# Optimization experiments

Measured on AMD Instinct MI355X. Metric: run time of the kernel, lower is better.

The kernel has to match this reference:

```python
import jax, jax.numpy as jnp
import numpy as np

N_TOK, D_MODEL, N_EXPERTS, TOP_K = 8192, 512, 8, 2


def setup_inputs() -> dict:
    key = jax.random.key(0)
    k1, k2, k3 = jax.random.split(key, 3)
    x = jax.random.normal(k1, (N_TOK, D_MODEL), jnp.float32)
    w_gate = jax.random.normal(k2, (D_MODEL, N_EXPERTS), jnp.float32) * 0.02
    expert_w = jax.random.normal(k3, (N_EXPERTS, D_MODEL, D_MODEL), jnp.float32) * (D_MODEL ** -0.5)
    return {"x": x, "w_gate": w_gate, "expert_w": expert_w, "top_k": TOP_K}


def _cv_sq(v):
    m = jnp.mean(v)
    return jnp.var(v) / (m * m + 1e-10)


def reference(x, w_gate, expert_w, top_k):
    # ---- Gate (clean top-k gating, eval mode of noisy-top-k) ----
    logits = x @ w_gate                              # [N, E]
    top_vals, top_idx = jax.lax.top_k(logits, top_k)  # [N, k]
    top_gates = jax.nn.softmax(top_vals, axis=-1)
    n, e = logits.shape
    gates = jnp.zeros((n, e), x.dtype).at[jnp.arange(n)[:, None], top_idx].set(top_gates)

    # ---- dispatch -> per-expert GEMM -> log-domain combine ----
    # combine(): stitched = cat(expert_out).exp() * nonzero_gates; index_add over
    # batch index; zeros -> eps; log. Dense-equivalent (tokens with gate 0
    # contribute exactly nothing):
    expert_out = jnp.einsum('nd,edf->nef', x, expert_w)   # per-expert outputs [N, E, D]
    combined = jnp.einsum('ne,nef->nf', gates, jnp.exp(expert_out))  # [N, D]
    eps = np.float32(np.finfo(np.float64).eps)
    combined = jnp.where(combined == 0, eps, combined)
    out = jnp.log(combined)

    # ---- load-balance aux loss: cv^2(importance) + cv^2(load) ----
    importance = gates.sum(0)
    load = (gates > 0).sum(0).astype(x.dtype)
    balance_loss = _cv_sq(importance) + _cv_sq(load)
    return out, balance_loss
```

## Files before the change

### kernel.cpp

```cpp
#include <hip/hip_runtime.h>
#include <hip/hip_bf16.h>
#include <math.h>

#define N_TOK 8192
#define D 512
#define NE 8

typedef float f32x4 __attribute__((ext_vector_type(4)));
typedef __bf16 bf16x8 __attribute__((ext_vector_type(8)));
typedef unsigned short u16;
typedef u16 u16x8 __attribute__((ext_vector_type(8)));

#define OFF_TOKG  65792
#define OFF_BUCK  131328
#define OFF_XB    (1u << 20)
#define OFF_EWT   (OFF_XB + 8u * 1024 * 1024)
#define OFF_Y     (OFF_EWT + 4u * 1024 * 1024)

__device__ __forceinline__ u16 f2b(float v) {
    __hip_bfloat16 h = __float2bfloat16(v);
    return *reinterpret_cast<u16*>(&h);
}
__device__ __forceinline__ float b2f(u16 u) {
    __hip_bfloat16 h;
    *reinterpret_cast<u16*>(&h) = u;
    return __bfloat162float(h);
}

typedef __attribute__((address_space(1))) const void* gp1_t;
typedef __attribute__((address_space(3))) void* lp3_t;
__device__ __forceinline__ void gload16(const void* g, void* l) {
    __builtin_amdgcn_global_load_lds((gp1_t)g, (lp3_t)l, 16, 0, 0);
}

__global__ __launch_bounds__(256) void gate_prep_kernel(
    const float* __restrict__ x, const float* __restrict__ wg,
    const float* __restrict__ ew,
    float* __restrict__ tok_g, u16* __restrict__ xb, u16* __restrict__ ewt,
    int* __restrict__ count, float* __restrict__ imp, int* __restrict__ bucket)
{
    __shared__ __align__(16) float sbuf[64 * 65];
    int b = blockIdx.x;
    int tid = threadIdx.x;

    if (b >= 512) {
        int pb = b - 512;
        float (*tile)[65] = (float(*)[65])sbuf;
        int e = pb >> 6, dt = (pb >> 3) & 7, ftl = pb & 7;
        int c = tid & 63, rq = tid >> 6;
        const float* src = ew + (size_t)e * D * D + (size_t)(dt * 64) * D + ftl * 64;
#pragma unroll
        for (int i = 0; i < 16; ++i) {
            int r = i * 4 + rq;
            tile[r][c] = src[(size_t)r * D + c];
        }
        __syncthreads();
        u16* dst = ewt + (size_t)e * D * D + (size_t)(ftl * 64) * D + dt * 64;
#pragma unroll
        for (int i = 0; i < 16; ++i) {
            int f = i * 4 + rq;
            dst[(size_t)f * D + c] = f2b(tile[c][f]);
        }
        return;
    }

    __shared__ int lcnt[NE], lbase[NE];
    __shared__ float limp[NE];
    __shared__ int se[32], so[32];
    if (tid < NE) { lcnt[tid] = 0; limp[tid] = 0.f; }

    float* wgs = sbuf;
    for (int i = tid; i < NE * D; i += 256) {
        int d = i >> 3, e = i & 7;
        wgs[e * D + d] = wg[i];
    }
    __syncthreads();

    int wave = tid >> 6, lane = tid & 63;
#pragma unroll
    for (int t = 0; t < 4; ++t) {
        int n = b * 16 + wave * 4 + t;
        const float4* xr4 = (const float4*)(x + (size_t)n * D);
        ushort4* xb4 = (ushort4*)(xb + (size_t)n * D);

        float p[NE];
#pragma unroll
        for (int e = 0; e < NE; ++e) p[e] = 0.f;
#pragma unroll
        for (int it = 0; it < 2; ++it) {
            float4 v = xr4[it * 64 + lane];
            ushort4 s;
            s.x = f2b(v.x); s.y = f2b(v.y); s.z = f2b(v.z); s.w = f2b(v.w);
            xb4[it * 64 + lane] = s;
#pragma unroll
            for (int e = 0; e < NE; ++e) {
                float4 wv = *(const float4*)&wgs[e * D + (it * 64 + lane) * 4];
                p[e] += v.x * wv.x + v.y * wv.y + v.z * wv.z + v.w * wv.w;
            }
        }
#pragma unroll
        for (int off = 32; off > 0; off >>= 1) {
#pragma unroll
            for (int e = 0; e < NE; ++e)
                p[e] += __shfl_xor(p[e], off);
        }

        if (lane == 0) {
            int e1 = 0; float v1 = p[0];
#pragma unroll
            for (int e = 1; e < NE; ++e) if (p[e] > v1) { v1 = p[e]; e1 = e; }
            int e2 = -1; float v2 = -INFINITY;
#pragma unroll
            for (int e = 0; e < NE; ++e) if (e != e1 && p[e] > v2) { v2 = p[e]; e2 = e; }
            float tv = __expf(v2 - v1);
            float inv = 1.f / (1.f + tv);
            float g1 = inv, g2 = tv * inv;
            tok_g[2 * n] = g1;    tok_g[2 * n + 1] = g2;
            int slot = wave * 4 + t;
            int o1 = atomicAdd(&lcnt[e1], 1);
            int o2 = atomicAdd(&lcnt[e2], 1);
            atomicAdd(&limp[e1], g1);
            atomicAdd(&limp[e2], g2);
            se[2 * slot] = e1;     so[2 * slot] = o1;
            se[2 * slot + 1] = e2; so[2 * slot + 1] = o2;
        }
    }
    __syncthreads();
    if (tid < NE) {
        lbase[tid] = atomicAdd(&count[tid], lcnt[tid]);
        atomicAdd(&imp[tid], limp[tid]);
    }
    __syncthreads();
    if (tid < 32) {
        int n = b * 16 + (tid >> 1);
        int e = se[tid];
        bucket[e * N_TOK + lbase[e] + so[tid]] = 2 * n + (tid & 1);
    }
}

__global__ __launch_bounds__(256) void moe_gemm(
    const u16* __restrict__ xb, const u16* __restrict__ ewt,
    const int* __restrict__ count, const int* __restrict__ bucket,
    u16* __restrict__ y)
{
    int b = blockIdx.x;
    int ft = b & 3;
    int tt = (b >> 2) & 63;
    int e  = b >> 8;
    int cnt = count[e];
    if (tt * 128 >= cnt) return;

    __shared__ int sl[128];
    __shared__ __align__(16) u16 smem[24576];

    int tid = threadIdx.x;
    if (tid < 128) {
        int idx = tt * 128 + tid;
        sl[tid] = (idx < cnt) ? bucket[e * N_TOK + idx] : -1;
    }
    __syncthreads();

    int w = tid >> 6, l = tid & 63;
    int c8 = (l & 3) * 8;
    int r0 = w * 32 + (l >> 2);
    int r1 = r0 + 16;
    int s0 = sl[r0], s1 = sl[r1];
    int ta0 = (s0 < 0) ? 0 : (s0 >> 1);
    int ta1 = (s1 < 0) ? 0 : (s1 >> 1);
    const u16* gA0 = xb + (size_t)ta0 * D + c8;
    const u16* gA1 = xb + (size_t)ta1 * D + c8;
    const u16* gB0 = ewt + ((size_t)e * D + ft * 128 + r0) * D + c8;
    const u16* gB1 = ewt + ((size_t)e * D + ft * 128 + r1) * D + c8;

    int wm = w & 1, wn = w >> 1;
    int lm = l & 15, quad = l >> 4, kq = quad * 8;

    f32x4 acc[4][4] = {};

    auto stage = [&](int p, int kc) {
        u16* As = smem + p * 8192;
        u16* Bs = As + 4096;
        gload16(gA0 + kc * 32, &As[(w * 32) * 32]);
        gload16(gA1 + kc * 32, &As[(w * 32 + 16) * 32]);
        gload16(gB0 + kc * 32, &Bs[(w * 32) * 32]);
        gload16(gB1 + kc * 32, &Bs[(w * 32 + 16) * 32]);
    };

    stage(0, 0);
    stage(1, 1);
    int bi = 0, bj = 2;
    for (int kc = 0; kc < 16; ++kc) {
        if (kc < 15)
            asm volatile("s_waitcnt vmcnt(4) lgkmcnt(0)" ::: "memory");
        else
            asm volatile("s_waitcnt vmcnt(0) lgkmcnt(0)" ::: "memory");
        __builtin_amdgcn_s_barrier();
        asm volatile("" ::: "memory");

        if (kc < 14) {
            stage(bj, kc + 2);
            bj = (bj == 2) ? 0 : bj + 1;
        }

        const u16* As = smem + bi * 8192;
        const u16* Bs = As + 4096;
        bi = (bi == 2) ? 0 : bi + 1;

        bf16x8 af[4], bfv[4];
#pragma unroll
        for (int i = 0; i < 4; ++i)
            af[i] = *(const bf16x8*)&As[(wm * 64 + i * 16 + lm) * 32 + kq];
#pragma unroll
        for (int j = 0; j < 4; ++j)
            bfv[j] = *(const bf16x8*)&Bs[(wn * 64 + j * 16 + lm) * 32 + kq];

        __builtin_amdgcn_s_setprio(1);
#pragma unroll
        for (int i = 0; i < 4; ++i)
#pragma unroll
            for (int j = 0; j < 4; ++j)
                acc[i][j] = __builtin_amdgcn_mfma_f32_16x16x32_bf16(
                    af[i], bfv[j], acc[i][j], 0, 0, 0);
        __builtin_amdgcn_s_setprio(0);
    }

    __syncthreads();
    u16* Es = smem + w * 2304;
#pragma unroll
    for (int h = 0; h < 2; ++h) {
#pragma unroll
        for (int i2 = 0; i2 < 2; ++i2) {
            int i = h * 2 + i2;
#pragma unroll
            for (int j = 0; j < 4; ++j)
#pragma unroll
                for (int r = 0; r < 4; ++r)
                    Es[(i2 * 16 + quad * 4 + r) * 72 + j * 16 + lm] =
                        f2b(acc[i][j][r]);
        }
        int row = l >> 1, hc = l & 1;
        int s = sl[wm * 64 + h * 32 + row];
        const u16* src = Es + row * 72 + hc * 32;
        u16* dst = y + (size_t)((s < 0) ? 0 : s) * D + ft * 128 + wn * 64 + hc * 32;
        if (s >= 0) {
#pragma unroll
            for (int c = 0; c < 4; ++c)
                *(u16x8*)(dst + c * 8) = *(const u16x8*)(src + c * 8);
        }
        __syncthreads();
    }
}

__global__ __launch_bounds__(256) void combine_kernel(
    const u16* __restrict__ y, const float* __restrict__ tok_g,
    const int* __restrict__ count, const float* __restrict__ imp,
    float* __restrict__ out)
{
    if (blockIdx.x == 2048) {
        if (threadIdx.x < 64) {
            int lane = threadIdx.x;
            float ci = (lane < NE) ? imp[lane] : 0.f;
            float cl = (lane < NE) ? (float)count[lane] : 0.f;
            float si = ci, sl2 = cl;
#pragma unroll
            for (int off = 4; off >= 1; off >>= 1) {
                si += __shfl_xor(si, off);
                sl2 += __shfl_xor(sl2, off);
            }
            float mi = si * 0.125f, ml = sl2 * 0.125f;
            float di = ci - mi, dl = cl - ml;
            float vi = (lane < NE) ? di * di : 0.f;
            float vl = (lane < NE) ? dl * dl : 0.f;
#pragma unroll
            for (int off = 4; off >= 1; off >>= 1) {
                vi += __shfl_xor(vi, off);
                vl += __shfl_xor(vl, off);
            }
            if (lane == 0) {
                vi *= 0.125f; vl *= 0.125f;
                out[N_TOK * D] = vi / (mi * mi + 1e-10f) + vl / (ml * ml + 1e-10f);
            }
        }
        return;
    }
    int idx = blockIdx.x * 256 + threadIdx.x;
    int n = idx >> 6;
    int c = (idx & 63) * 8;
    const u16x8 ua = *(const u16x8*)(y + (size_t)(2 * n) * D + c);
    const u16x8 ub = *(const u16x8*)(y + (size_t)(2 * n + 1) * D + c);
    float g1 = tok_g[2 * n], g2 = tok_g[2 * n + 1];
    const float eps = 2.2204460492503131e-16f;
    float r[8];
#pragma unroll
    for (int k = 0; k < 8; ++k) {
        float v = g1 * __expf(b2f(ua[k])) + g2 * __expf(b2f(ub[k]));
        r[k] = __logf(v == 0.f ? eps : v);
    }
    float* o = out + (size_t)n * D + c;
    *(float4*)o       = make_float4(r[0], r[1], r[2], r[3]);
    *(float4*)(o + 4) = make_float4(r[4], r[5], r[6], r[7]);
}

extern "C" void kernel_launch(void* const* d_in, const int* in_sizes, int n_in,
                              void* d_out, int out_size, void* d_ws, size_t ws_size,
                              hipStream_t stream)
{
    const float* x  = (const float*)d_in[0];
    const float* wg = (const float*)d_in[1];
    const float* ew = (const float*)d_in[2];
    char* ws = (char*)d_ws;
    int*   count  = (int*)(ws + 0);
    float* imp    = (float*)(ws + 64);
    float* tok_g  = (float*)(ws + OFF_TOKG);
    int*   bucket = (int*)(ws + OFF_BUCK);
    u16*   xb     = (u16*)(ws + OFF_XB);
    u16*   ewt    = (u16*)(ws + OFF_EWT);
    u16*   y      = (u16*)(ws + OFF_Y);
    float* out    = (float*)d_out;

    hipMemsetAsync(ws, 0, 128, stream);
    gate_prep_kernel<<<512 + 512, 256, 0, stream>>>(x, wg, ew, tok_g, xb, ewt,
                                                    count, imp, bucket);
    moe_gemm<<<NE * 64 * 4, 256, 0, stream>>>(xb, ewt, count, bucket, y);
    combine_kernel<<<2049, 256, 0, stream>>>(y, tok_g, count, imp, out);
}
```

Baseline: 125.5 us.

## Fuse gate, GEMM and combine into one cooperative persistent kernel with grid syncs

Replaces the three separate launches (gate/prep, per-expert GEMM, combine) with a single cooperative persistent kernel. It loops over work units in each phase and separates the phases with grid.sync(). The aim is to remove the launch overhead and tail gaps between kernels. The grid is sized from the occupancy query, capped at 2048 blocks, and the old launches remain as a fallback. The costs are grid-wide barriers and the register and occupancy limits of one fused kernel.

```diff
diff --git a/kernel.cpp b/kernel.cpp
--- a/kernel.cpp
+++ b/kernel.cpp
@@ -1,6 +1,9 @@
 #include <hip/hip_runtime.h>
+#include <hip/hip_cooperative_groups.h>
 #include <hip/hip_bf16.h>
 #include <math.h>
+
+namespace cg = cooperative_groups;
 
 #define N_TOK 8192
 #define D 512
@@ -31,6 +34,273 @@
 typedef __attribute__((address_space(3))) void* lp3_t;
 __device__ __forceinline__ void gload16(const void* g, void* l) {
     __builtin_amdgcn_global_load_lds((gp1_t)g, (lp3_t)l, 16, 0, 0);
+}
+
+__global__ __launch_bounds__(256, 3) void moe_mega(
+    const float* __restrict__ x, const float* __restrict__ wg,
+    const float* __restrict__ ew,
+    float* __restrict__ tok_g, u16* __restrict__ xb, u16* __restrict__ ewt,
+    int* __restrict__ count, float* __restrict__ imp, int* __restrict__ bucket,
+    u16* __restrict__ y, float* __restrict__ out)
+{
+    cg::grid_group grid = cg::this_grid();
+    const int tid = threadIdx.x;
+    const int G = gridDim.x;
+
+    __shared__ __align__(16) u16 smem[24576];
+    __shared__ int sl[128];
+    __shared__ int lcnt[NE], lbase[NE];
+    __shared__ float limp[NE];
+    __shared__ int se[32], so[32];
+
+    const int w = tid >> 6, l = tid & 63;
+
+    for (int u = blockIdx.x; u < 768; u += G) {
+        __syncthreads();
+        if (u < 512) {
+            float* wgs = (float*)smem;
+            if (tid < NE) { lcnt[tid] = 0; limp[tid] = 0.f; }
+            for (int i = tid; i < NE * D; i += 256) {
+                int d = i >> 3, e = i & 7;
+                wgs[e * D + d] = wg[i];
+            }
+            __syncthreads();
+
+#pragma unroll
+            for (int t = 0; t < 4; ++t) {
+                int n = u * 16 + w * 4 + t;
+                const float4* xr4 = (const float4*)(x + (size_t)n * D);
+                ushort4* xb4 = (ushort4*)(xb + (size_t)n * D);
+
+                float p[NE];
+#pragma unroll
+                for (int e = 0; e < NE; ++e) p[e] = 0.f;
+#pragma unroll
+                for (int it = 0; it < 2; ++it) {
+                    float4 v = xr4[it * 64 + l];
+                    ushort4 s;
+                    s.x = f2b(v.x); s.y = f2b(v.y); s.z = f2b(v.z); s.w = f2b(v.w);
+                    xb4[it * 64 + l] = s;
+#pragma unroll
+                    for (int e = 0; e < NE; ++e) {
+                        float4 wv = *(const float4*)&wgs[e * D + (it * 64 + l) * 4];
+                        p[e] += v.x * wv.x + v.y * wv.y + v.z * wv.z + v.w * wv.w;
+                    }
+                }
+#pragma unroll
+                for (int off = 32; off > 0; off >>= 1) {
+#pragma unroll
+                    for (int e = 0; e < NE; ++e)
+                        p[e] += __shfl_xor(p[e], off);
+                }
+
+                if (l == 0) {
+                    int e1 = 0; float v1 = p[0];
+#pragma unroll
+                    for (int e = 1; e < NE; ++e) if (p[e] > v1) { v1 = p[e]; e1 = e; }
+                    int e2 = -1; float v2 = -INFINITY;
+#pragma unroll
+                    for (int e = 0; e < NE; ++e) if (e != e1 && p[e] > v2) { v2 = p[e]; e2 = e; }
+                    float tv = __expf(v2 - v1);
+                    float inv = 1.f / (1.f + tv);
+                    float g1 = inv, g2 = tv * inv;
+                    tok_g[2 * n] = g1;    tok_g[2 * n + 1] = g2;
+                    int slot = w * 4 + t;
+                    int o1 = atomicAdd(&lcnt[e1], 1);
+                    int o2 = atomicAdd(&lcnt[e2], 1);
+                    atomicAdd(&limp[e1], g1);
+                    atomicAdd(&limp[e2], g2);
+                    se[2 * slot] = e1;     so[2 * slot] = o1;
+                    se[2 * slot + 1] = e2; so[2 * slot + 1] = o2;
+                }
+            }
+            __syncthreads();
+            if (tid < NE) {
+                lbase[tid] = atomicAdd(&count[tid], lcnt[tid]);
+                atomicAdd(&imp[tid], limp[tid]);
+            }
+            __syncthreads();
+            if (tid < 32) {
+                int n = u * 16 + (tid >> 1);
+                int e = se[tid];
+                bucket[e * N_TOK + lbase[e] + so[tid]] = 2 * n + (tid & 1);
+            }
+        } else {
+            float (*tile)[65] = (float(*)[65])smem;
+            int c = tid & 63, rq = tid >> 6;
+#pragma unroll
+            for (int half = 0; half < 2; ++half) {
+                int pb = (u - 512) * 2 + half;
+                int e = pb >> 6, dt = (pb >> 3) & 7, ftl = pb & 7;
+                const float* src = ew + (size_t)e * D * D + (size_t)(dt * 64) * D + ftl * 64;
+#pragma unroll
+                for (int i = 0; i < 16; ++i) {
+                    int r = i * 4 + rq;
+                    tile[r][c] = src[(size_t)r * D + c];
+                }
+                __syncthreads();
+                u16* dst = ewt + (size_t)e * D * D + (size_t)(ftl * 64) * D + dt * 64;
+#pragma unroll
+                for (int i = 0; i < 16; ++i) {
+                    int f = i * 4 + rq;
+                    dst[(size_t)f * D + c] = f2b(tile[c][f]);
+                }
+                __syncthreads();
+            }
+        }
+    }
+
+    grid.sync();
+
+    {
+        const int c8 = (l & 3) * 8;
+        const int wm = w & 1, wn = w >> 1;
+        const int lm = l & 15, quad = l >> 4, kq = quad * 8;
+
+        for (int u = blockIdx.x; u < 2048; u += G) {
+            int e = u & 7, ft = (u >> 3) & 3, tt = u >> 5;
+            int cnt = count[e];
+            if (tt * 128 >= cnt) continue;
+
+            if (tid < 128) {
+                int idx = tt * 128 + tid;
+                sl[tid] = (idx < cnt) ? bucket[e * N_TOK + idx] : -1;
+            }
+            __syncthreads();
+
+            int r0 = w * 32 + (l >> 2);
+            int r1 = r0 + 16;
+            int s0 = sl[r0], s1 = sl[r1];
+            int ta0 = (s0 < 0) ? 0 : (s0 >> 1);
+            int ta1 = (s1 < 0) ? 0 : (s1 >> 1);
+            const u16* gA0 = xb + (size_t)ta0 * D + c8;
+            const u16* gA1 = xb + (size_t)ta1 * D + c8;
+            const u16* gB0 = ewt + ((size_t)e * D + ft * 128 + r0) * D + c8;
+            const u16* gB1 = ewt + ((size_t)e * D + ft * 128 + r1) * D + c8;
+
+            f32x4 acc[4][4] = {};
+
+            auto stage = [&](int p, int kc) {
+                u16* As = smem + p * 8192;
+                u16* Bs = As + 4096;
+                gload16(gA0 + kc * 32, &As[(w * 32) * 32]);
+                gload16(gA1 + kc * 32, &As[(w * 32 + 16) * 32]);
+                gload16(gB0 + kc * 32, &Bs[(w * 32) * 32]);
+                gload16(gB1 + kc * 32, &Bs[(w * 32 + 16) * 32]);
+            };
+
+            stage(0, 0);
+            stage(1, 1);
+            int bi = 0, bj = 2;
+            for (int kc = 0; kc < 16; ++kc) {
+                if (kc < 15)
+                    asm volatile("s_waitcnt vmcnt(4) lgkmcnt(0)" ::: "memory");
+                else
+                    asm volatile("s_waitcnt vmcnt(0) lgkmcnt(0)" ::: "memory");
+                __builtin_amdgcn_s_barrier();
+                asm volatile("" ::: "memory");
+
+                if (kc < 14) {
+                    stage(bj, kc + 2);
+                    bj = (bj == 2) ? 0 : bj + 1;
+                }
+
+                const u16* As = smem + bi * 8192;
+                const u16* Bs = As + 4096;
+                bi = (bi == 2) ? 0 : bi + 1;
+
+                bf16x8 af[4], bfv[4];
+#pragma unroll
+                for (int i = 0; i < 4; ++i)
+                    af[i] = *(const bf16x8*)&As[(wm * 64 + i * 16 + lm) * 32 + kq];
+#pragma unroll
+                for (int j = 0; j < 4; ++j)
+                    bfv[j] = *(const bf16x8*)&Bs[(wn * 64 + j * 16 + lm) * 32 + kq];
+
+                __builtin_amdgcn_s_setprio(1);
+#pragma unroll
+                for (int i = 0; i < 4; ++i)
+#pragma unroll
+                    for (int j = 0; j < 4; ++j)
+                        acc[i][j] = __builtin_amdgcn_mfma_f32_16x16x32_bf16(
+                            af[i], bfv[j], acc[i][j], 0, 0, 0);
+                __builtin_amdgcn_s_setprio(0);
+            }
+
+            __syncthreads();
+            u16* Es = smem + w * 2304;
+#pragma unroll
+            for (int h = 0; h < 2; ++h) {
+#pragma unroll
+                for (int i2 = 0; i2 < 2; ++i2) {
+                    int i = h * 2 + i2;
+#pragma unroll
+                    for (int j = 0; j < 4; ++j)
+#pragma unroll
+                        for (int r = 0; r < 4; ++r)
+                            Es[(i2 * 16 + quad * 4 + r) * 72 + j * 16 + lm] =
+                                f2b(acc[i][j][r]);
+                }
+                int row = l >> 1, hc = l & 1;
+                int s = sl[wm * 64 + h * 32 + row];
+                const u16* src = Es + row * 72 + hc * 32;
+                u16* dst = y + (size_t)((s < 0) ? 0 : s) * D + ft * 128 + wn * 64 + hc * 32;
+                if (s >= 0) {
+#pragma unroll
+                    for (int c = 0; c < 4; ++c)
+                        *(u16x8*)(dst + c * 8) = *(const u16x8*)(src + c * 8);
+                }
+                __syncthreads();
+            }
+        }
+    }
+
+    grid.sync();
+
+    for (int u = blockIdx.x; u < 2049; u += G) {
+        if (u == 2048) {
+            if (tid < 64) {
+                float ci = (tid < NE) ? imp[tid] : 0.f;
+                float cl = (tid < NE) ? (float)count[tid] : 0.f;
+                float si = ci, sl2 = cl;
+#pragma unroll
+                for (int off = 4; off >= 1; off >>= 1) {
+                    si += __shfl_xor(si, off);
+                    sl2 += __shfl_xor(sl2, off);
+                }
+                float mi = si * 0.125f, ml = sl2 * 0.125f;
+                float di = ci - mi, dl = cl - ml;
+                float vi = (tid < NE) ? di * di : 0.f;
+                float vl = (tid < NE) ? dl * dl : 0.f;
+#pragma unroll
+                for (int off = 4; off >= 1; off >>= 1) {
+                    vi += __shfl_xor(vi, off);
+                    vl += __shfl_xor(vl, off);
+                }
+                if (tid == 0) {
+                    vi *= 0.125f; vl *= 0.125f;
+                    out[N_TOK * D] = vi / (mi * mi + 1e-10f) + vl / (ml * ml + 1e-10f);
+                }
+            }
+            continue;
+        }
+        int idx = u * 256 + tid;
+        int n = idx >> 6;
+        int c = (idx & 63) * 8;
+        const u16x8 ua = *(const u16x8*)(y + (size_t)(2 * n) * D + c);
+        const u16x8 ub = *(const u16x8*)(y + (size_t)(2 * n + 1) * D + c);
+        float g1 = tok_g[2 * n], g2 = tok_g[2 * n + 1];
+        const float eps = 2.2204460492503131e-16f;
+        float r[8];
+#pragma unroll
+        for (int k = 0; k < 8; ++k) {
+            float v = g1 * __expf(b2f(ua[k])) + g2 * __expf(b2f(ub[k]));
+            r[k] = __logf(v == 0.f ? eps : v);
+        }
+        float* o = out + (size_t)n * D + c;
+        *(float4*)o       = make_float4(r[0], r[1], r[2], r[3]);
+        *(float4*)(o + 4) = make_float4(r[4], r[5], r[6], r[7]);
+    }
 }
 
 __global__ __launch_bounds__(256) void gate_prep_kernel(
@@ -319,8 +589,32 @@
     float* out    = (float*)d_out;
 
     hipMemsetAsync(ws, 0, 128, stream);
-    gate_prep_kernel<<<512 + 512, 256, 0, stream>>>(x, wg, ew, tok_g, xb, ewt,
-                                                    count, imp, bucket);
-    moe_gemm<<<NE * 64 * 4, 256, 0, stream>>>(xb, ewt, count, bucket, y);
-    combine_kernel<<<2049, 256, 0, stream>>>(y, tok_g, count, imp, out);
-}
+
+    static int coopBlocks = -1;
+    if (coopBlocks < 0) {
+        int nb = 0;
+        if (hipOccupancyMaxActiveBlocksPerMultiprocessor(&nb, moe_mega, 256, 0)
+                != hipSuccess || nb < 1)
+            nb = 0;
+        coopBlocks = nb;
+    }
+
+    bool launched = false;
+    if (coopBlocks >= 1) {
+        int G = coopBlocks * 256;
+        if (G > 2048) G = 2048;
+        void* args[] = {(void*)&x, (void*)&wg, (void*)&ew, (void*)&tok_g,
+                        (void*)&xb, (void*)&ewt, (void*)&count, (void*)&imp,
+                        (void*)&bucket, (void*)&y, (void*)&out};
+        if (hipLaunchCooperativeKernel(moe_mega, dim3(G), dim3(256),
+                                       args, 0u, stream) == hipSuccess)
+            launched = true;
+    }
+
+    if (!launched) {
+        gate_prep_kernel<<<512 + 512, 256, 0, stream>>>(x, wg, ew, tok_g, xb, ewt,
+                                                        count, imp, bucket);
+        moe_gemm<<<NE * 64 * 4, 256, 0, stream>>>(xb, ewt, count, bucket, y);
+        combine_kernel<<<2049, 256, 0, stream>>>(y, tok_g, count, imp, out);
+    }
+}
```

Result: slower. 230.2 us (+83.5%).
